# Optimization experiments

Hardware: AMD Instinct MI355X
Metric: run time of the kernel (lower is better)

The kernel has to match this reference:

```python
import jax, jax.numpy as jnp
import numpy as np

D = 2048      # d_model
E = 8         # total experts (0 old + 8 new)
R = 16        # adapter rank
K = 2         # top_k
INIT_BONUS = 3.0
ANNEAL_STEPS = 5000
CURRENT_STEP = 1  # first forward call increments the buffer from 0 to 1


def setup_inputs() -> dict:
    key = jax.random.key(0)
    ks = jax.random.split(key, 7)
    s_in = 1.0 / np.sqrt(D)
    s_r = 1.0 / np.sqrt(R)
    return {
        "x": jax.random.normal(ks[0], (2, 4096, D), dtype=jnp.float32),
        "Wr": jax.random.normal(ks[1], (D, E), dtype=jnp.float32) * s_in,   # router weight
        "br": jax.random.normal(ks[2], (E,), dtype=jnp.float32) * 0.01,     # router bias
        "Wd": jax.random.normal(ks[3], (E, D, R), dtype=jnp.float32) * s_in,  # per-expert down proj
        "bd": jnp.zeros((E, R), dtype=jnp.float32),
        "Wu": jax.random.normal(ks[4], (E, R, D), dtype=jnp.float32) * s_r,   # per-expert up proj
        "bu": jnp.zeros((E, D), dtype=jnp.float32),
    }


def reference(x, Wr, br, Wd, bd, Wu, bu):
    # Router
    logits = jnp.einsum('btd,de->bte', x, Wr) + br
    # Boosted logits (mode='train'): all E experts are new (old_expert_count=0),
    # so the bonus is added to every logit (softmax-invariant here, kept for fidelity).
    progress = min(CURRENT_STEP / ANNEAL_STEPS, 1.0)
    bonus = INIT_BONUS * (1.0 - progress)
    logits = logits + bonus
    gates = jax.nn.softmax(logits, axis=-1)                      # [B,T,E]
    topk_vals, topk_idx = jax.lax.top_k(gates, K)                # [B,T,K]
    topk_vals = topk_vals / topk_vals.sum(axis=-1, keepdims=True)
    # Per-token combine weight for each expert (0 if not in top-k) -- equals the
    # torch loop's weight = (topk_vals * (topk_idx == e)).sum(-1)
    w = (jax.nn.one_hot(topk_idx, E, dtype=x.dtype) * topk_vals[..., None]).sum(axis=-2)  # [B,T,E]
    # Dense per-expert adapter (faithful to the source's dense loop):
    # Adapter(x) = relu(x @ Wd + bd) @ Wu + bu
    h = jax.nn.relu(jnp.einsum('btd,edr->betr', x, Wd) + bd[None, :, None, :])  # [B,E,T,R]
    eo = jnp.einsum('betr,erd->betd', h, Wu) + bu[None, :, None, :]             # [B,E,T,D]
    # Weighted accumulate: output = sum_e w[...,e] * expert_out_e
    out = jnp.einsum('bte,betd->btd', w, eo)                                    # [B,T,D]
    return out
```

## Files before the change

kernel.cpp:

```cpp
#include <hip/hip_runtime.h>
#include <math.h>

#define DMODEL 2048
#define NEXP   8
#define RANK   16
#define NPAIR  28
#define MAXT16 576
#define MAXT32 320

__global__ __launch_bounds__(256, 2)
void router_kernel(const float* __restrict__ x,
                   const float* __restrict__ Wr,
                   const float* __restrict__ br,
                   float2* __restrict__ wparams,
                   int* __restrict__ cnt,
                   unsigned short* __restrict__ lists,
                   int nTok)
{
    __shared__ float wr_lds[DMODEL * NEXP];
    const int tid = threadIdx.x;
    #pragma unroll
    for (int i = 0; i < 16; ++i) {
        const int f = (i*256 + tid)*4;
        *(float4*)&wr_lds[f] = *(const float4*)&Wr[f];
    }
    __syncthreads();

    const int s = tid >> 3;
    const int j = tid & 7;
    const int tok = blockIdx.x*32 + s;
    const bool valid = tok < nTok;
    const float* xr = x + (size_t)(valid ? tok : 0) * DMODEL;

    float part[NEXP];
    #pragma unroll
    for (int e = 0; e < NEXP; ++e) part[e] = 0.f;

    for (int i = 0; i < 64; ++i) {
        const int d0 = (i*8 + j)*4;
        const float4 xv = *(const float4*)&xr[d0];
        #pragma unroll
        for (int q = 0; q < 4; ++q) {
            const float xq = (q==0)?xv.x:(q==1)?xv.y:(q==2)?xv.z:xv.w;
            const float4 w0 = *(const float4*)&wr_lds[(d0+q)*NEXP];
            const float4 w1 = *(const float4*)&wr_lds[(d0+q)*NEXP + 4];
            part[0] = fmaf(xq, w0.x, part[0]);
            part[1] = fmaf(xq, w0.y, part[1]);
            part[2] = fmaf(xq, w0.z, part[2]);
            part[3] = fmaf(xq, w0.w, part[3]);
            part[4] = fmaf(xq, w1.x, part[4]);
            part[5] = fmaf(xq, w1.y, part[5]);
            part[6] = fmaf(xq, w1.z, part[6]);
            part[7] = fmaf(xq, w1.w, part[7]);
        }
    }
    #pragma unroll
    for (int mres = 1; mres < 8; mres <<= 1) {
        #pragma unroll
        for (int e = 0; e < NEXP; ++e)
            part[e] += __shfl_xor(part[e], mres);
    }

    if (j == 0 && valid) {
        float lg[NEXP];
        #pragma unroll
        for (int e = 0; e < NEXP; ++e) lg[e] = part[e] + br[e];
        int b0 = 0; float v0 = lg[0];
        #pragma unroll
        for (int e = 1; e < NEXP; ++e) { if (lg[e] > v0) { v0 = lg[e]; b0 = e; } }
        int b1 = (b0 == 0) ? 1 : 0; float v1 = lg[b1];
        #pragma unroll
        for (int e = 0; e < NEXP; ++e) { if (e != b0 && lg[e] > v1) { v1 = lg[e]; b1 = e; } }
        const float t = expf(v1 - v0);
        const float wtop = 1.f / (1.f + t);
        const float wsec = t / (1.f + t);
        const int lo = (b0 < b1) ? b0 : b1;
        const int hi = (b0 < b1) ? b1 : b0;
        const float wlo = (b0 < b1) ? wtop : wsec;
        const float whi = (b0 < b1) ? wsec : wtop;
        wparams[tok] = make_float2(wlo, whi);
        const int pidx = lo*(NEXP-1) - (lo*(lo-1))/2 + (hi - lo - 1);
        const int pos = atomicAdd(&cnt[pidx], 1);
        lists[(size_t)pidx*nTok + pos] = (unsigned short)tok;
    }
}

__global__ void prefix_kernel(const int* __restrict__ cnt,
                              int* __restrict__ to16,
                              int* __restrict__ to32)
{
    if (threadIdx.x == 0) {
        int a16 = 0, a32 = 0;
        for (int p = 0; p < NPAIR; ++p) {
            to16[p] = a16; to32[p] = a32;
            a16 += (cnt[p] + 15) >> 4;
            a32 += (cnt[p] + 31) >> 5;
        }
        to16[NPAIR] = a16; to32[NPAIR] = a32;
    }
}

__global__ __launch_bounds__(256, 2)
void down_kernel(const float* __restrict__ x,
                 const float* __restrict__ Wd,
                 const float* __restrict__ bd,
                 const float2* __restrict__ wparams,
                 const int* __restrict__ cnt,
                 const int* __restrict__ to16,
                 const unsigned short* __restrict__ lists,
                 float* __restrict__ hw,
                 int nTok)
{
    const int bx = blockIdx.x;
    if (bx >= to16[NPAIR]) return;
    int p = 0;
    while (to16[p+1] <= bx) ++p;
    const int tile = bx - to16[p];
    const int m = min(16, cnt[p] - tile*16);
    int lo = 0, rem = p;
    while (rem >= (NEXP-1-lo)) { rem -= (NEXP-1-lo); ++lo; }
    const int hi = lo + 1 + rem;

    __shared__ float x_lds[16][132];
    __shared__ float wd_lds[2][128][20];
    __shared__ float w_lds[2][16];
    __shared__ int   tok_lds[16];

    const int tid = threadIdx.x;
    if (tid < 16) {
        const int idx = tile*16 + ((tid < m) ? tid : 0);
        const int t = lists[(size_t)p*nTok + idx];
        tok_lds[tid] = t;
        const float2 w = wparams[t];
        w_lds[0][tid] = (tid < m) ? w.x : 0.f;
        w_lds[1][tid] = (tid < m) ? w.y : 0.f;
    }
    __syncthreads();

    const int dg = tid & 31;
    const int kq = tid >> 5;
    const int k  = kq >> 2;
    const int tq = kq & 3;
    const int e  = k ? hi : lo;

    const int sA = tid >> 4;
    const int bA = tid & 15;
    const size_t xbase = (size_t)tok_lds[sA]*DMODEL + bA*8;

    float acc[4][16];
    #pragma unroll
    for (int i = 0; i < 4; ++i)
        #pragma unroll
        for (int r = 0; r < 16; ++r) acc[i][r] = 0.f;

    for (int c = 0; c < 16; ++c) {
        if (c) __syncthreads();
        *(float4*)&x_lds[sA][bA*8]     = *(const float4*)&x[xbase + c*128];
        *(float4*)&x_lds[sA][bA*8 + 4] = *(const float4*)&x[xbase + c*128 + 4];
        #pragma unroll
        for (int o = 0; o < 4; ++o) {
            const int f  = tid*16 + o*4;
            const int kk = f >> 11;
            const int f2 = f & 2047;
            const int es = kk ? hi : lo;
            *(float4*)&wd_lds[kk][f2 >> 4][f2 & 15] =
                *(const float4*)&Wd[(size_t)es*(DMODEL*RANK) + (size_t)c*2048 + f2];
        }
        __syncthreads();
        #pragma unroll
        for (int j = 0; j < 4; ++j) {
            const int d = j*32 + dg;
            const float4 wa = *(const float4*)&wd_lds[k][d][0];
            const float4 wb = *(const float4*)&wd_lds[k][d][4];
            const float4 wc = *(const float4*)&wd_lds[k][d][8];
            const float4 we = *(const float4*)&wd_lds[k][d][12];
            #pragma unroll
            for (int i = 0; i < 4; ++i) {
                const float xv = x_lds[tq*4 + i][d];
                acc[i][0]  = fmaf(xv, wa.x, acc[i][0]);
                acc[i][1]  = fmaf(xv, wa.y, acc[i][1]);
                acc[i][2]  = fmaf(xv, wa.z, acc[i][2]);
                acc[i][3]  = fmaf(xv, wa.w, acc[i][3]);
                acc[i][4]  = fmaf(xv, wb.x, acc[i][4]);
                acc[i][5]  = fmaf(xv, wb.y, acc[i][5]);
                acc[i][6]  = fmaf(xv, wb.z, acc[i][6]);
                acc[i][7]  = fmaf(xv, wb.w, acc[i][7]);
                acc[i][8]  = fmaf(xv, wc.x, acc[i][8]);
                acc[i][9]  = fmaf(xv, wc.y, acc[i][9]);
                acc[i][10] = fmaf(xv, wc.z, acc[i][10]);
                acc[i][11] = fmaf(xv, wc.w, acc[i][11]);
                acc[i][12] = fmaf(xv, we.x, acc[i][12]);
                acc[i][13] = fmaf(xv, we.y, acc[i][13]);
                acc[i][14] = fmaf(xv, we.z, acc[i][14]);
                acc[i][15] = fmaf(xv, we.w, acc[i][15]);
            }
        }
    }

    #pragma unroll
    for (int mm = 1; mm <= 16; mm <<= 1)
        #pragma unroll
        for (int i = 0; i < 4; ++i)
            #pragma unroll
            for (int r = 0; r < 16; ++r)
                acc[i][r] += __shfl_xor(acc[i][r], mm);

    if (dg == 0) {
        #pragma unroll
        for (int i = 0; i < 4; ++i) {
            const int slot = tq*4 + i;
            if (slot < m) {
                const int t = tok_lds[slot];
                const float w = w_lds[k][slot];
                float4 h0, h1, h2, h3;
                h0.x = fmaxf(acc[i][0]  + bd[e*RANK+0],  0.f) * w;
                h0.y = fmaxf(acc[i][1]  + bd[e*RANK+1],  0.f) * w;
                h0.z = fmaxf(acc[i][2]  + bd[e*RANK+2],  0.f) * w;
                h0.w = fmaxf(acc[i][3]  + bd[e*RANK+3],  0.f) * w;
                h1.x = fmaxf(acc[i][4]  + bd[e*RANK+4],  0.f) * w;
                h1.y = fmaxf(acc[i][5]  + bd[e*RANK+5],  0.f) * w;
                h1.z = fmaxf(acc[i][6]  + bd[e*RANK+6],  0.f) * w;
                h1.w = fmaxf(acc[i][7]  + bd[e*RANK+7],  0.f) * w;
                h2.x = fmaxf(acc[i][8]  + bd[e*RANK+8],  0.f) * w;
                h2.y = fmaxf(acc[i][9]  + bd[e*RANK+9],  0.f) * w;
                h2.z = fmaxf(acc[i][10] + bd[e*RANK+10], 0.f) * w;
                h2.w = fmaxf(acc[i][11] + bd[e*RANK+11], 0.f) * w;
                h3.x = fmaxf(acc[i][12] + bd[e*RANK+12], 0.f) * w;
                h3.y = fmaxf(acc[i][13] + bd[e*RANK+13], 0.f) * w;
                h3.z = fmaxf(acc[i][14] + bd[e*RANK+14], 0.f) * w;
                h3.w = fmaxf(acc[i][15] + bd[e*RANK+15], 0.f) * w;
                float* hp = &hw[(size_t)t*32 + k*16];
                *(float4*)&hp[0]  = h0;
                *(float4*)&hp[4]  = h1;
                *(float4*)&hp[8]  = h2;
                *(float4*)&hp[12] = h3;
            }
        }
    }
}

__global__ __launch_bounds__(256, 2)
void up_kernel(const float* __restrict__ Wu,
               const float* __restrict__ bu,
               const float2* __restrict__ wparams,
               const int* __restrict__ cnt,
               const int* __restrict__ to32,
               const unsigned short* __restrict__ lists,
               const float* __restrict__ hw,
               float* __restrict__ out,
               int nTok)
{
    const int bx = blockIdx.x;
    if (bx >= to32[NPAIR]) return;
    int p = 0;
    while (to32[p+1] <= bx) ++p;
    const int tile = bx - to32[p];
    const int m = min(32, cnt[p] - tile*32);
    int lo = 0, rem = p;
    while (rem >= (NEXP-1-lo)) { rem -= (NEXP-1-lo); ++lo; }
    const int hi = lo + 1 + rem;
    const int cc = blockIdx.y;

    __shared__ float wu_lds[2][16][256];
    __shared__ float h_lds[32][36];
    __shared__ float w2_lds[2][32];
    __shared__ int   tok_lds[32];

    const int tid = threadIdx.x;

    if (tid < 32) {
        const int idx = tile*32 + ((tid < m) ? tid : 0);
        const int t = lists[(size_t)p*nTok + idx];
        tok_lds[tid] = t;
        const float2 w = wparams[t];
        w2_lds[0][tid] = (tid < m) ? w.x : 0.f;
        w2_lds[1][tid] = (tid < m) ? w.y : 0.f;
    }

    #pragma unroll
    for (int i = 0; i < 8; ++i) {
        const int f  = i*1024 + tid*4;
        const int kk = f >> 12;
        const int rr = (f >> 8) & 15;
        const int dd = f & 255;
        const int es = kk ? hi : lo;
        *(float4*)&wu_lds[kk][rr][dd] =
            *(const float4*)&Wu[(size_t)es*(RANK*DMODEL) + (size_t)rr*DMODEL + cc*256 + dd];
    }
    __syncthreads();

    {
        const int tk = tid >> 3, o = (tid & 7) * 4;
        const float4 hv = *(const float4*)&hw[(size_t)tok_lds[tk]*32 + o];
        *(float4*)&h_lds[tk][o] = hv;
    }
    __syncthreads();

    const int dg = tid & 31;
    const int tq = tid >> 5;
    float4 a0[4], a1[4];
    #pragma unroll
    for (int i = 0; i < 4; ++i) { a0[i] = make_float4(0,0,0,0); a1[i] = make_float4(0,0,0,0); }

    #pragma unroll 8
    for (int kr = 0; kr < 32; ++kr) {
        const int kk = kr >> 4, rr = kr & 15;
        const float4 u0 = *(const float4*)&wu_lds[kk][rr][dg*4];
        const float4 u1 = *(const float4*)&wu_lds[kk][rr][128 + dg*4];
        #pragma unroll
        for (int i = 0; i < 4; ++i) {
            const float hv = h_lds[tq*4 + i][kr];
            a0[i].x = fmaf(hv, u0.x, a0[i].x);
            a0[i].y = fmaf(hv, u0.y, a0[i].y);
            a0[i].z = fmaf(hv, u0.z, a0[i].z);
            a0[i].w = fmaf(hv, u0.w, a0[i].w);
            a1[i].x = fmaf(hv, u1.x, a1[i].x);
            a1[i].y = fmaf(hv, u1.y, a1[i].y);
            a1[i].z = fmaf(hv, u1.z, a1[i].z);
            a1[i].w = fmaf(hv, u1.w, a1[i].w);
        }
    }

    const float4 bl0 = *(const float4*)&bu[(size_t)lo*DMODEL + cc*256 + dg*4];
    const float4 bl1 = *(const float4*)&bu[(size_t)lo*DMODEL + cc*256 + 128 + dg*4];
    const float4 bh0 = *(const float4*)&bu[(size_t)hi*DMODEL + cc*256 + dg*4];
    const float4 bh1 = *(const float4*)&bu[(size_t)hi*DMODEL + cc*256 + 128 + dg*4];

    #pragma unroll
    for (int i = 0; i < 4; ++i) {
        const int slot = tq*4 + i;
        if (slot < m) {
            const int t = tok_lds[slot];
            const float wl = w2_lds[0][slot];
            const float wh = w2_lds[1][slot];
            float4 o0 = a0[i], o1 = a1[i];
            o0.x += wl*bl0.x + wh*bh0.x;  o0.y += wl*bl0.y + wh*bh0.y;
            o0.z += wl*bl0.z + wh*bh0.z;  o0.w += wl*bl0.w + wh*bh0.w;
            o1.x += wl*bl1.x + wh*bh1.x;  o1.y += wl*bl1.y + wh*bh1.y;
            o1.z += wl*bl1.z + wh*bh1.z;  o1.w += wl*bl1.w + wh*bh1.w;
            float* op = &out[(size_t)t*DMODEL + cc*256];
            *(float4*)&op[dg*4]       = o0;
            *(float4*)&op[128 + dg*4] = o1;
        }
    }
}

extern "C" void kernel_launch(void* const* d_in, const int* in_sizes, int n_in,
                              void* d_out, int out_size, void* d_ws, size_t ws_size,
                              hipStream_t stream)
{
    (void)n_in; (void)out_size; (void)ws_size;
    const float* x  = (const float*)d_in[0];
    const float* Wr = (const float*)d_in[1];
    const float* br = (const float*)d_in[2];
    const float* Wd = (const float*)d_in[3];
    const float* bd = (const float*)d_in[4];
    const float* Wu = (const float*)d_in[5];
    const float* bu = (const float*)d_in[6];
    float* out = (float*)d_out;
    const int nTok = in_sizes[0] / DMODEL;

    char* base = (char*)d_ws;
    int* cnt  = (int*)(base);
    int* to16 = (int*)(base + 128);
    int* to32 = (int*)(base + 256);
    float2* wparams = (float2*)(base + 512);
    size_t off = 512 + (size_t)nTok*sizeof(float2);
    unsigned short* lists = (unsigned short*)(base + off);
    off += (size_t)NPAIR*nTok*sizeof(unsigned short);
    off = (off + 255) & ~(size_t)255;
    float* hw = (float*)(base + off);

    hipMemsetAsync(d_ws, 0, 512, stream);
    const int ntiles = (nTok + 31)/32;
    router_kernel<<<ntiles, 256, 0, stream>>>(x, Wr, br, wparams, cnt, lists, nTok);
    prefix_kernel<<<1, 64, 0, stream>>>(cnt, to16, to32);
    down_kernel<<<MAXT16, 256, 0, stream>>>(x, Wd, bd, wparams, cnt, to16, lists, hw, nTok);
    dim3 gup(MAXT32, 8);
    up_kernel<<<gup, 256, 0, stream>>>(Wu, bu, wparams, cnt, to32, lists, hw, out, nTok);
}
```

Before: 111.6 us.

## Rewrite down projection as per-thread token dot products and transpose router weights

The down-projection kernel drops its LDS-tiled 16-token scheme with cross-lane shuffle reductions. Each thread now owns one token, one expert of the pair and four rank outputs, streaming its x row and Wd directly from global memory over 32-token tiles. The router transposes Wr into an expert-major LDS layout and has each thread handle two tokens, so each weight read is reused across both. This removes LDS staging, barriers and the large shuffle reduction, at the cost of uncoalesced per-thread x row reads and heavy L1/L2 reliance.

Result: slower. 308.9 us (+176.8%).

```diff
diff --git a/kernel.cpp b/kernel.cpp
--- a/kernel.cpp
+++ b/kernel.cpp
@@ -5,7 +5,6 @@
 #define NEXP   8
 #define RANK   16
 #define NPAIR  28
-#define MAXT16 576
 #define MAXT32 320
 
 __global__ __launch_bounds__(256, 2)
@@ -17,86 +16,98 @@
                    unsigned short* __restrict__ lists,
                    int nTok)
 {
-    __shared__ float wr_lds[DMODEL * NEXP];
+    __shared__ float wr_t[NEXP][DMODEL];
     const int tid = threadIdx.x;
     #pragma unroll
     for (int i = 0; i < 16; ++i) {
         const int f = (i*256 + tid)*4;
-        *(float4*)&wr_lds[f] = *(const float4*)&Wr[f];
+        const int d = f >> 3;
+        const int e0 = f & 7;
+        const float4 v = *(const float4*)&Wr[f];
+        wr_t[e0+0][d] = v.x;
+        wr_t[e0+1][d] = v.y;
+        wr_t[e0+2][d] = v.z;
+        wr_t[e0+3][d] = v.w;
     }
     __syncthreads();
 
-    const int s = tid >> 3;
-    const int j = tid & 7;
-    const int tok = blockIdx.x*32 + s;
-    const bool valid = tok < nTok;
-    const float* xr = x + (size_t)(valid ? tok : 0) * DMODEL;
-
-    float part[NEXP];
-    #pragma unroll
-    for (int e = 0; e < NEXP; ++e) part[e] = 0.f;
-
-    for (int i = 0; i < 64; ++i) {
-        const int d0 = (i*8 + j)*4;
-        const float4 xv = *(const float4*)&xr[d0];
+    const int j  = tid & 15;
+    const int su = tid >> 4;
+    const int tok0 = blockIdx.x*32 + su*2;
+    const int tok1 = tok0 + 1;
+    const bool v0 = tok0 < nTok, v1 = tok1 < nTok;
+    const float* xr0 = x + (size_t)(v0 ? tok0 : 0) * DMODEL;
+    const float* xr1 = x + (size_t)(v1 ? tok1 : 0) * DMODEL;
+
+    float pa[NEXP], pb[NEXP];
+    #pragma unroll
+    for (int e = 0; e < NEXP; ++e) { pa[e] = 0.f; pb[e] = 0.f; }
+
+    for (int i = 0; i < 32; ++i) {
+        const int d0 = (i*16 + j)*4;
+        const float4 xa = *(const float4*)&xr0[d0];
+        const float4 xb = *(const float4*)&xr1[d0];
         #pragma unroll
-        for (int q = 0; q < 4; ++q) {
-            const float xq = (q==0)?xv.x:(q==1)?xv.y:(q==2)?xv.z:xv.w;
-            const float4 w0 = *(const float4*)&wr_lds[(d0+q)*NEXP];
-            const float4 w1 = *(const float4*)&wr_lds[(d0+q)*NEXP + 4];
-            part[0] = fmaf(xq, w0.x, part[0]);
-            part[1] = fmaf(xq, w0.y, part[1]);
-            part[2] = fmaf(xq, w0.z, part[2]);
-            part[3] = fmaf(xq, w0.w, part[3]);
-            part[4] = fmaf(xq, w1.x, part[4]);
-            part[5] = fmaf(xq, w1.y, part[5]);
-            part[6] = fmaf(xq, w1.z, part[6]);
-            part[7] = fmaf(xq, w1.w, part[7]);
-        }
-    }
-    #pragma unroll
-    for (int mres = 1; mres < 8; mres <<= 1) {
+        for (int e = 0; e < NEXP; ++e) {
+            const float4 wv = *(const float4*)&wr_t[e][d0];
+            pa[e] = fmaf(xa.x, wv.x, pa[e]);
+            pa[e] = fmaf(xa.y, wv.y, pa[e]);
+            pa[e] = fmaf(xa.z, wv.z, pa[e]);
+            pa[e] = fmaf(xa.w, wv.w, pa[e]);
+            pb[e] = fmaf(xb.x, wv.x, pb[e]);
+            pb[e] = fmaf(xb.y, wv.y, pb[e]);
+            pb[e] = fmaf(xb.z, wv.z, pb[e]);
+            pb[e] = fmaf(xb.w, wv.w, pb[e]);
+        }
+    }
+    #pragma unroll
+    for (int mres = 1; mres < 16; mres <<= 1) {
         #pragma unroll
-        for (int e = 0; e < NEXP; ++e)
-            part[e] += __shfl_xor(part[e], mres);
-    }
-
-    if (j == 0 && valid) {
-        float lg[NEXP];
+        for (int e = 0; e < NEXP; ++e) {
+            pa[e] += __shfl_xor(pa[e], mres);
+            pb[e] += __shfl_xor(pb[e], mres);
+        }
+    }
+
+    if (j == 0) {
         #pragma unroll
-        for (int e = 0; e < NEXP; ++e) lg[e] = part[e] + br[e];
-        int b0 = 0; float v0 = lg[0];
-        #pragma unroll
-        for (int e = 1; e < NEXP; ++e) { if (lg[e] > v0) { v0 = lg[e]; b0 = e; } }
-        int b1 = (b0 == 0) ? 1 : 0; float v1 = lg[b1];
-        #pragma unroll
-        for (int e = 0; e < NEXP; ++e) { if (e != b0 && lg[e] > v1) { v1 = lg[e]; b1 = e; } }
-        const float t = expf(v1 - v0);
-        const float wtop = 1.f / (1.f + t);
-        const float wsec = t / (1.f + t);
-        const int lo = (b0 < b1) ? b0 : b1;
-        const int hi = (b0 < b1) ? b1 : b0;
-        const float wlo = (b0 < b1) ? wtop : wsec;
-        const float whi = (b0 < b1) ? wsec : wtop;
-        wparams[tok] = make_float2(wlo, whi);
-        const int pidx = lo*(NEXP-1) - (lo*(lo-1))/2 + (hi - lo - 1);
-        const int pos = atomicAdd(&cnt[pidx], 1);
-        lists[(size_t)pidx*nTok + pos] = (unsigned short)tok;
+        for (int tt = 0; tt < 2; ++tt) {
+            const int tok = tt ? tok1 : tok0;
+            if (tok >= nTok) continue;
+            float lg[NEXP];
+            #pragma unroll
+            for (int e = 0; e < NEXP; ++e) lg[e] = (tt ? pb[e] : pa[e]) + br[e];
+            int b0 = 0; float w0 = lg[0];
+            #pragma unroll
+            for (int e = 1; e < NEXP; ++e) { if (lg[e] > w0) { w0 = lg[e]; b0 = e; } }
+            int b1 = (b0 == 0) ? 1 : 0; float w1 = lg[b1];
+            #pragma unroll
+            for (int e = 0; e < NEXP; ++e) { if (e != b0 && lg[e] > w1) { w1 = lg[e]; b1 = e; } }
+            const float t = expf(w1 - w0);
+            const float wtop = 1.f / (1.f + t);
+            const float wsec = t / (1.f + t);
+            const int lo = (b0 < b1) ? b0 : b1;
+            const int hi = (b0 < b1) ? b1 : b0;
+            const float wlo = (b0 < b1) ? wtop : wsec;
+            const float whi = (b0 < b1) ? wsec : wtop;
+            wparams[tok] = make_float2(wlo, whi);
+            const int pidx = lo*(NEXP-1) - (lo*(lo-1))/2 + (hi - lo - 1);
+            const int pos = atomicAdd(&cnt[pidx], 1);
+            lists[(size_t)pidx*nTok + pos] = (unsigned short)tok;
+        }
     }
 }
 
 __global__ void prefix_kernel(const int* __restrict__ cnt,
-                              int* __restrict__ to16,
                               int* __restrict__ to32)
 {
     if (threadIdx.x == 0) {
-        int a16 = 0, a32 = 0;
+        int a32 = 0;
         for (int p = 0; p < NPAIR; ++p) {
-            to16[p] = a16; to32[p] = a32;
-            a16 += (cnt[p] + 15) >> 4;
+            to32[p] = a32;
             a32 += (cnt[p] + 31) >> 5;
         }
-        to16[NPAIR] = a16; to32[NPAIR] = a32;
+        to32[NPAIR] = a32;
     }
 }
 
@@ -105,137 +116,62 @@
                  const float* __restrict__ Wd,
                  const float* __restrict__ bd,
                  const float2* __restrict__ wparams,
+                 const int* __restrict__ to32,
                  const int* __restrict__ cnt,
-                 const int* __restrict__ to16,
                  const unsigned short* __restrict__ lists,
                  float* __restrict__ hw,
                  int nTok)
 {
     const int bx = blockIdx.x;
-    if (bx >= to16[NPAIR]) return;
+    if (bx >= to32[NPAIR]) return;
     int p = 0;
-    while (to16[p+1] <= bx) ++p;
-    const int tile = bx - to16[p];
-    const int m = min(16, cnt[p] - tile*16);
+    while (to32[p+1] <= bx) ++p;
+    const int tile = bx - to32[p];
+    const int m = min(32, cnt[p] - tile*32);
     int lo = 0, rem = p;
     while (rem >= (NEXP-1-lo)) { rem -= (NEXP-1-lo); ++lo; }
     const int hi = lo + 1 + rem;
 
-    __shared__ float x_lds[16][132];
-    __shared__ float wd_lds[2][128][20];
-    __shared__ float w_lds[2][16];
-    __shared__ int   tok_lds[16];
-
     const int tid = threadIdx.x;
-    if (tid < 16) {
-        const int idx = tile*16 + ((tid < m) ? tid : 0);
-        const int t = lists[(size_t)p*nTok + idx];
-        tok_lds[tid] = t;
-        const float2 w = wparams[t];
-        w_lds[0][tid] = (tid < m) ? w.x : 0.f;
-        w_lds[1][tid] = (tid < m) ? w.y : 0.f;
-    }
-    __syncthreads();
-
-    const int dg = tid & 31;
-    const int kq = tid >> 5;
-    const int k  = kq >> 2;
-    const int tq = kq & 3;
+    const int ts = tid & 31;
+    const int k  = (tid >> 5) & 1;
+    const int rq = tid >> 6;
     const int e  = k ? hi : lo;
-
-    const int sA = tid >> 4;
-    const int bA = tid & 15;
-    const size_t xbase = (size_t)tok_lds[sA]*DMODEL + bA*8;
-
-    float acc[4][16];
-    #pragma unroll
-    for (int i = 0; i < 4; ++i)
-        #pragma unroll
-        for (int r = 0; r < 16; ++r) acc[i][r] = 0.f;
-
-    for (int c = 0; c < 16; ++c) {
-        if (c) __syncthreads();
-        *(float4*)&x_lds[sA][bA*8]     = *(const float4*)&x[xbase + c*128];
-        *(float4*)&x_lds[sA][bA*8 + 4] = *(const float4*)&x[xbase + c*128 + 4];
-        #pragma unroll
-        for (int o = 0; o < 4; ++o) {
-            const int f  = tid*16 + o*4;
-            const int kk = f >> 11;
-            const int f2 = f & 2047;
-            const int es = kk ? hi : lo;
-            *(float4*)&wd_lds[kk][f2 >> 4][f2 & 15] =
-                *(const float4*)&Wd[(size_t)es*(DMODEL*RANK) + (size_t)c*2048 + f2];
-        }
-        __syncthreads();
-        #pragma unroll
-        for (int j = 0; j < 4; ++j) {
-            const int d = j*32 + dg;
-            const float4 wa = *(const float4*)&wd_lds[k][d][0];
-            const float4 wb = *(const float4*)&wd_lds[k][d][4];
-            const float4 wc = *(const float4*)&wd_lds[k][d][8];
-            const float4 we = *(const float4*)&wd_lds[k][d][12];
-            #pragma unroll
-            for (int i = 0; i < 4; ++i) {
-                const float xv = x_lds[tq*4 + i][d];
-                acc[i][0]  = fmaf(xv, wa.x, acc[i][0]);
-                acc[i][1]  = fmaf(xv, wa.y, acc[i][1]);
-                acc[i][2]  = fmaf(xv, wa.z, acc[i][2]);
-                acc[i][3]  = fmaf(xv, wa.w, acc[i][3]);
-                acc[i][4]  = fmaf(xv, wb.x, acc[i][4]);
-                acc[i][5]  = fmaf(xv, wb.y, acc[i][5]);
-                acc[i][6]  = fmaf(xv, wb.z, acc[i][6]);
-                acc[i][7]  = fmaf(xv, wb.w, acc[i][7]);
-                acc[i][8]  = fmaf(xv, wc.x, acc[i][8]);
-                acc[i][9]  = fmaf(xv, wc.y, acc[i][9]);
-                acc[i][10] = fmaf(xv, wc.z, acc[i][10]);
-                acc[i][11] = fmaf(xv, wc.w, acc[i][11]);
-                acc[i][12] = fmaf(xv, we.x, acc[i][12]);
-                acc[i][13] = fmaf(xv, we.y, acc[i][13]);
-                acc[i][14] = fmaf(xv, we.z, acc[i][14]);
-                acc[i][15] = fmaf(xv, we.w, acc[i][15]);
-            }
-        }
-    }
-
-    #pragma unroll
-    for (int mm = 1; mm <= 16; mm <<= 1)
-        #pragma unroll
-        for (int i = 0; i < 4; ++i)
-            #pragma unroll
-            for (int r = 0; r < 16; ++r)
-                acc[i][r] += __shfl_xor(acc[i][r], mm);
-
-    if (dg == 0) {
-        #pragma unroll
-        for (int i = 0; i < 4; ++i) {
-            const int slot = tq*4 + i;
-            if (slot < m) {
-                const int t = tok_lds[slot];
-                const float w = w_lds[k][slot];
-                float4 h0, h1, h2, h3;
-                h0.x = fmaxf(acc[i][0]  + bd[e*RANK+0],  0.f) * w;
-                h0.y = fmaxf(acc[i][1]  + bd[e*RANK+1],  0.f) * w;
-                h0.z = fmaxf(acc[i][2]  + bd[e*RANK+2],  0.f) * w;
-                h0.w = fmaxf(acc[i][3]  + bd[e*RANK+3],  0.f) * w;
-                h1.x = fmaxf(acc[i][4]  + bd[e*RANK+4],  0.f) * w;
-                h1.y = fmaxf(acc[i][5]  + bd[e*RANK+5],  0.f) * w;
-                h1.z = fmaxf(acc[i][6]  + bd[e*RANK+6],  0.f) * w;
-                h1.w = fmaxf(acc[i][7]  + bd[e*RANK+7],  0.f) * w;
-                h2.x = fmaxf(acc[i][8]  + bd[e*RANK+8],  0.f) * w;
-                h2.y = fmaxf(acc[i][9]  + bd[e*RANK+9],  0.f) * w;
-                h2.z = fmaxf(acc[i][10] + bd[e*RANK+10], 0.f) * w;
-                h2.w = fmaxf(acc[i][11] + bd[e*RANK+11], 0.f) * w;
-                h3.x = fmaxf(acc[i][12] + bd[e*RANK+12], 0.f) * w;
-                h3.y = fmaxf(acc[i][13] + bd[e*RANK+13], 0.f) * w;
-                h3.z = fmaxf(acc[i][14] + bd[e*RANK+14], 0.f) * w;
-                h3.w = fmaxf(acc[i][15] + bd[e*RANK+15], 0.f) * w;
-                float* hp = &hw[(size_t)t*32 + k*16];
-                *(float4*)&hp[0]  = h0;
-                *(float4*)&hp[4]  = h1;
-                *(float4*)&hp[8]  = h2;
-                *(float4*)&hp[12] = h3;
-            }
-        }
+    const bool valid = ts < m;
+    const int tok = lists[(size_t)p*nTok + tile*32 + (valid ? ts : 0)];
+
+    const float* xp = x + (size_t)tok * DMODEL;
+    const float* wp = Wd + (size_t)e * (DMODEL*RANK) + rq*4;
+
+    float ax = 0.f, ay = 0.f, az = 0.f, aw = 0.f;
+    #pragma unroll 4
+    for (int dc = 0; dc < DMODEL/4; ++dc) {
+        const int d = dc*4;
+        const float4 xv = *(const float4*)&xp[d];
+        const float4 w0 = *(const float4*)&wp[(d+0)*RANK];
+        const float4 w1 = *(const float4*)&wp[(d+1)*RANK];
+        const float4 w2 = *(const float4*)&wp[(d+2)*RANK];
+        const float4 w3 = *(const float4*)&wp[(d+3)*RANK];
+        ax = fmaf(xv.x, w0.x, ax); ax = fmaf(xv.y, w1.x, ax);
+        ax = fmaf(xv.z, w2.x, ax); ax = fmaf(xv.w, w3.x, ax);
+        ay = fmaf(xv.x, w0.y, ay); ay = fmaf(xv.y, w1.y, ay);
+        ay = fmaf(xv.z, w2.y, ay); ay = fmaf(xv.w, w3.y, ay);
+        az = fmaf(xv.x, w0.z, az); az = fmaf(xv.y, w1.z, az);
+        az = fmaf(xv.z, w2.z, az); az = fmaf(xv.w, w3.z, az);
+        aw = fmaf(xv.x, w0.w, aw); aw = fmaf(xv.y, w1.w, aw);
+        aw = fmaf(xv.z, w2.w, aw); aw = fmaf(xv.w, w3.w, aw);
+    }
+
+    const float2 wp2 = wparams[tok];
+    const float w = k ? wp2.y : wp2.x;
+    const float4 bdv = *(const float4*)&bd[e*RANK + rq*4];
+    float4 h;
+    h.x = fmaxf(ax + bdv.x, 0.f) * w;
+    h.y = fmaxf(ay + bdv.y, 0.f) * w;
+    h.z = fmaxf(az + bdv.z, 0.f) * w;
+    h.w = fmaxf(aw + bdv.w, 0.f) * w;
+    if (valid) {
+        *(float4*)&hw[(size_t)tok*32 + k*16 + rq*4] = h;
     }
 }
 
@@ -362,7 +298,6 @@
 
     char* base = (char*)d_ws;
     int* cnt  = (int*)(base);
-    int* to16 = (int*)(base + 128);
     int* to32 = (int*)(base + 256);
     float2* wparams = (float2*)(base + 512);
     size_t off = 512 + (size_t)nTok*sizeof(float2);
@@ -374,8 +309,8 @@
     hipMemsetAsync(d_ws, 0, 512, stream);
     const int ntiles = (nTok + 31)/32;
     router_kernel<<<ntiles, 256, 0, stream>>>(x, Wr, br, wparams, cnt, lists, nTok);
-    prefix_kernel<<<1, 64, 0, stream>>>(cnt, to16, to32);
-    down_kernel<<<MAXT16, 256, 0, stream>>>(x, Wd, bd, wparams, cnt, to16, lists, hw, nTok);
+    prefix_kernel<<<1, 64, 0, stream>>>(cnt, to32);
+    down_kernel<<<MAXT32, 256, 0, stream>>>(x, Wd, bd, wparams, to32, cnt, lists, hw, nTok);
     dim3 gup(MAXT32, 8);
     up_kernel<<<gup, 256, 0, stream>>>(Wu, bu, wparams, cnt, to32, lists, hw, out, nTok);
 }
```

## Restructure router and split down-projection over two D halves

Applied to the files above, without the earlier changes.

The router drops its 64KB LDS staging of Wr. Each block now handles 16 tokens, each warp-group covers two experts, and Wr and x are read straight from global memory. The down kernel adds a grid dimension that splits D into two halves and reads x and Wd directly without LDS tiles or barriers, writing partial sums to a wider hw2 buffer. The up kernel then adds the two partials, applies bias, ReLU and the gate weight. The aim is more parallelism and occupancy in the router and down stages; the cost is uncoalesced scalar x gathers and extra partial-sum traffic.

Measured after the change: 149.4 us. 33.9% more time.

```diff
diff --git a/kernel.cpp b/kernel.cpp
--- a/kernel.cpp
+++ b/kernel.cpp
@@ -17,71 +17,76 @@
                    unsigned short* __restrict__ lists,
                    int nTok)
 {
-    __shared__ float wr_lds[DMODEL * NEXP];
+    __shared__ float lg_lds[16][8];
+
     const int tid = threadIdx.x;
-    #pragma unroll
-    for (int i = 0; i < 16; ++i) {
-        const int f = (i*256 + tid)*4;
-        *(float4*)&wr_lds[f] = *(const float4*)&Wr[f];
+    const int dg  = tid & 31;
+    const int grp = tid >> 5;
+    const int ep  = grp & 3;
+    const int th  = grp >> 2;
+    const int tbase = blockIdx.x*16 + th*8;
+
+    float a0[8], a1[8];
+    #pragma unroll
+    for (int t = 0; t < 8; ++t) { a0[t] = 0.f; a1[t] = 0.f; }
+
+    for (int it = 0; it < 16; ++it) {
+        const int d0 = it*128 + dg*4;
+        const float2 w0 = *(const float2*)&Wr[(d0+0)*NEXP + ep*2];
+        const float2 w1 = *(const float2*)&Wr[(d0+1)*NEXP + ep*2];
+        const float2 w2 = *(const float2*)&Wr[(d0+2)*NEXP + ep*2];
+        const float2 w3 = *(const float2*)&Wr[(d0+3)*NEXP + ep*2];
+        #pragma unroll
+        for (int t = 0; t < 8; ++t) {
+            const float4 xv = *(const float4*)&x[(size_t)(tbase+t)*DMODEL + d0];
+            a0[t] = fmaf(xv.x, w0.x, a0[t]);
+            a0[t] = fmaf(xv.y, w1.x, a0[t]);
+            a0[t] = fmaf(xv.z, w2.x, a0[t]);
+            a0[t] = fmaf(xv.w, w3.x, a0[t]);
+            a1[t] = fmaf(xv.x, w0.y, a1[t]);
+            a1[t] = fmaf(xv.y, w1.y, a1[t]);
+            a1[t] = fmaf(xv.z, w2.y, a1[t]);
+            a1[t] = fmaf(xv.w, w3.y, a1[t]);
+        }
+    }
+    #pragma unroll
+    for (int mm = 1; mm <= 16; mm <<= 1) {
+        #pragma unroll
+        for (int t = 0; t < 8; ++t) {
+            a0[t] += __shfl_xor(a0[t], mm);
+            a1[t] += __shfl_xor(a1[t], mm);
+        }
+    }
+    if (dg < 8) {
+        lg_lds[th*8 + dg][ep*2 + 0] = a0[dg];
+        lg_lds[th*8 + dg][ep*2 + 1] = a1[dg];
     }
     __syncthreads();
 
-    const int s = tid >> 3;
-    const int j = tid & 7;
-    const int tok = blockIdx.x*32 + s;
-    const bool valid = tok < nTok;
-    const float* xr = x + (size_t)(valid ? tok : 0) * DMODEL;
-
-    float part[NEXP];
-    #pragma unroll
-    for (int e = 0; e < NEXP; ++e) part[e] = 0.f;
-
-    for (int i = 0; i < 64; ++i) {
-        const int d0 = (i*8 + j)*4;
-        const float4 xv = *(const float4*)&xr[d0];
-        #pragma unroll
-        for (int q = 0; q < 4; ++q) {
-            const float xq = (q==0)?xv.x:(q==1)?xv.y:(q==2)?xv.z:xv.w;
-            const float4 w0 = *(const float4*)&wr_lds[(d0+q)*NEXP];
-            const float4 w1 = *(const float4*)&wr_lds[(d0+q)*NEXP + 4];
-            part[0] = fmaf(xq, w0.x, part[0]);
-            part[1] = fmaf(xq, w0.y, part[1]);
-            part[2] = fmaf(xq, w0.z, part[2]);
-            part[3] = fmaf(xq, w0.w, part[3]);
-            part[4] = fmaf(xq, w1.x, part[4]);
-            part[5] = fmaf(xq, w1.y, part[5]);
-            part[6] = fmaf(xq, w1.z, part[6]);
-            part[7] = fmaf(xq, w1.w, part[7]);
-        }
-    }
-    #pragma unroll
-    for (int mres = 1; mres < 8; mres <<= 1) {
-        #pragma unroll
-        for (int e = 0; e < NEXP; ++e)
-            part[e] += __shfl_xor(part[e], mres);
-    }
-
-    if (j == 0 && valid) {
-        float lg[NEXP];
-        #pragma unroll
-        for (int e = 0; e < NEXP; ++e) lg[e] = part[e] + br[e];
-        int b0 = 0; float v0 = lg[0];
-        #pragma unroll
-        for (int e = 1; e < NEXP; ++e) { if (lg[e] > v0) { v0 = lg[e]; b0 = e; } }
-        int b1 = (b0 == 0) ? 1 : 0; float v1 = lg[b1];
-        #pragma unroll
-        for (int e = 0; e < NEXP; ++e) { if (e != b0 && lg[e] > v1) { v1 = lg[e]; b1 = e; } }
-        const float t = expf(v1 - v0);
-        const float wtop = 1.f / (1.f + t);
-        const float wsec = t / (1.f + t);
-        const int lo = (b0 < b1) ? b0 : b1;
-        const int hi = (b0 < b1) ? b1 : b0;
-        const float wlo = (b0 < b1) ? wtop : wsec;
-        const float whi = (b0 < b1) ? wsec : wtop;
-        wparams[tok] = make_float2(wlo, whi);
-        const int pidx = lo*(NEXP-1) - (lo*(lo-1))/2 + (hi - lo - 1);
-        const int pos = atomicAdd(&cnt[pidx], 1);
-        lists[(size_t)pidx*nTok + pos] = (unsigned short)tok;
+    if (tid < 16) {
+        const int tok = blockIdx.x*16 + tid;
+        if (tok < nTok) {
+            float lg[NEXP];
+            #pragma unroll
+            for (int e = 0; e < NEXP; ++e) lg[e] = lg_lds[tid][e] + br[e];
+            int b0 = 0; float v0 = lg[0];
+            #pragma unroll
+            for (int e = 1; e < NEXP; ++e) { if (lg[e] > v0) { v0 = lg[e]; b0 = e; } }
+            int b1 = (b0 == 0) ? 1 : 0; float v1 = lg[b1];
+            #pragma unroll
+            for (int e = 0; e < NEXP; ++e) { if (e != b0 && lg[e] > v1) { v1 = lg[e]; b1 = e; } }
+            const float t = expf(v1 - v0);
+            const float wtop = 1.f / (1.f + t);
+            const float wsec = t / (1.f + t);
+            const int lo = (b0 < b1) ? b0 : b1;
+            const int hi = (b0 < b1) ? b1 : b0;
+            const float wlo = (b0 < b1) ? wtop : wsec;
+            const float whi = (b0 < b1) ? wsec : wtop;
+            wparams[tok] = make_float2(wlo, whi);
+            const int pidx = lo*(NEXP-1) - (lo*(lo-1))/2 + (hi - lo - 1);
+            const int pos = atomicAdd(&cnt[pidx], 1);
+            lists[(size_t)pidx*nTok + pos] = (unsigned short)tok;
+        }
     }
 }
 
@@ -103,12 +108,10 @@
 __global__ __launch_bounds__(256, 2)
 void down_kernel(const float* __restrict__ x,
                  const float* __restrict__ Wd,
-                 const float* __restrict__ bd,
-                 const float2* __restrict__ wparams,
                  const int* __restrict__ cnt,
                  const int* __restrict__ to16,
                  const unsigned short* __restrict__ lists,
-                 float* __restrict__ hw,
+                 float* __restrict__ hw2,
                  int nTok)
 {
     const int bx = blockIdx.x;
@@ -120,32 +123,22 @@
     int lo = 0, rem = p;
     while (rem >= (NEXP-1-lo)) { rem -= (NEXP-1-lo); ++lo; }
     const int hi = lo + 1 + rem;
-
-    __shared__ float x_lds[16][132];
-    __shared__ float wd_lds[2][128][20];
-    __shared__ float w_lds[2][16];
-    __shared__ int   tok_lds[16];
+    const int ch = blockIdx.y;
 
     const int tid = threadIdx.x;
-    if (tid < 16) {
-        const int idx = tile*16 + ((tid < m) ? tid : 0);
-        const int t = lists[(size_t)p*nTok + idx];
-        tok_lds[tid] = t;
-        const float2 w = wparams[t];
-        w_lds[0][tid] = (tid < m) ? w.x : 0.f;
-        w_lds[1][tid] = (tid < m) ? w.y : 0.f;
-    }
-    __syncthreads();
-
     const int dg = tid & 31;
-    const int kq = tid >> 5;
-    const int k  = kq >> 2;
-    const int tq = kq & 3;
+    const int tq = (tid >> 5) & 3;
+    const int k  = tid >> 7;
     const int e  = k ? hi : lo;
 
-    const int sA = tid >> 4;
-    const int bA = tid & 15;
-    const size_t xbase = (size_t)tok_lds[sA]*DMODEL + bA*8;
+    int toks[4];
+    #pragma unroll
+    for (int i = 0; i < 4; ++i) {
+        const int slot = tq*4 + i;
+        toks[i] = lists[(size_t)p*nTok + tile*16 + ((slot < m) ? slot : 0)];
+    }
+
+    const float* wdp = Wd + (size_t)e * (DMODEL*RANK);
 
     float acc[4][16];
     #pragma unroll
@@ -153,47 +146,35 @@
         #pragma unroll
         for (int r = 0; r < 16; ++r) acc[i][r] = 0.f;
 
-    for (int c = 0; c < 16; ++c) {
-        if (c) __syncthreads();
-        *(float4*)&x_lds[sA][bA*8]     = *(const float4*)&x[xbase + c*128];
-        *(float4*)&x_lds[sA][bA*8 + 4] = *(const float4*)&x[xbase + c*128 + 4];
-        #pragma unroll
-        for (int o = 0; o < 4; ++o) {
-            const int f  = tid*16 + o*4;
-            const int kk = f >> 11;
-            const int f2 = f & 2047;
-            const int es = kk ? hi : lo;
-            *(float4*)&wd_lds[kk][f2 >> 4][f2 & 15] =
-                *(const float4*)&Wd[(size_t)es*(DMODEL*RANK) + (size_t)c*2048 + f2];
-        }
-        __syncthreads();
-        #pragma unroll
-        for (int j = 0; j < 4; ++j) {
-            const int d = j*32 + dg;
-            const float4 wa = *(const float4*)&wd_lds[k][d][0];
-            const float4 wb = *(const float4*)&wd_lds[k][d][4];
-            const float4 wc = *(const float4*)&wd_lds[k][d][8];
-            const float4 we = *(const float4*)&wd_lds[k][d][12];
-            #pragma unroll
-            for (int i = 0; i < 4; ++i) {
-                const float xv = x_lds[tq*4 + i][d];
-                acc[i][0]  = fmaf(xv, wa.x, acc[i][0]);
-                acc[i][1]  = fmaf(xv, wa.y, acc[i][1]);
-                acc[i][2]  = fmaf(xv, wa.z, acc[i][2]);
-                acc[i][3]  = fmaf(xv, wa.w, acc[i][3]);
-                acc[i][4]  = fmaf(xv, wb.x, acc[i][4]);
-                acc[i][5]  = fmaf(xv, wb.y, acc[i][5]);
-                acc[i][6]  = fmaf(xv, wb.z, acc[i][6]);
-                acc[i][7]  = fmaf(xv, wb.w, acc[i][7]);
-                acc[i][8]  = fmaf(xv, wc.x, acc[i][8]);
-                acc[i][9]  = fmaf(xv, wc.y, acc[i][9]);
-                acc[i][10] = fmaf(xv, wc.z, acc[i][10]);
-                acc[i][11] = fmaf(xv, wc.w, acc[i][11]);
-                acc[i][12] = fmaf(xv, we.x, acc[i][12]);
-                acc[i][13] = fmaf(xv, we.y, acc[i][13]);
-                acc[i][14] = fmaf(xv, we.z, acc[i][14]);
-                acc[i][15] = fmaf(xv, we.w, acc[i][15]);
-            }
+    const int dbase = ch*1024 + dg;
+    #pragma unroll 2
+    for (int jj = 0; jj < 32; ++jj) {
+        const int d = dbase + jj*32;
+        const float4 w0 = *(const float4*)&wdp[d*RANK + 0];
+        const float4 w1 = *(const float4*)&wdp[d*RANK + 4];
+        const float4 w2 = *(const float4*)&wdp[d*RANK + 8];
+        const float4 w3 = *(const float4*)&wdp[d*RANK + 12];
+        float xv[4];
+        #pragma unroll
+        for (int i = 0; i < 4; ++i) xv[i] = x[(size_t)toks[i]*DMODEL + d];
+        #pragma unroll
+        for (int i = 0; i < 4; ++i) {
+            acc[i][0]  = fmaf(xv[i], w0.x, acc[i][0]);
+            acc[i][1]  = fmaf(xv[i], w0.y, acc[i][1]);
+            acc[i][2]  = fmaf(xv[i], w0.z, acc[i][2]);
+            acc[i][3]  = fmaf(xv[i], w0.w, acc[i][3]);
+            acc[i][4]  = fmaf(xv[i], w1.x, acc[i][4]);
+            acc[i][5]  = fmaf(xv[i], w1.y, acc[i][5]);
+            acc[i][6]  = fmaf(xv[i], w1.z, acc[i][6]);
+            acc[i][7]  = fmaf(xv[i], w1.w, acc[i][7]);
+            acc[i][8]  = fmaf(xv[i], w2.x, acc[i][8]);
+            acc[i][9]  = fmaf(xv[i], w2.y, acc[i][9]);
+            acc[i][10] = fmaf(xv[i], w2.z, acc[i][10]);
+            acc[i][11] = fmaf(xv[i], w2.w, acc[i][11]);
+            acc[i][12] = fmaf(xv[i], w3.x, acc[i][12]);
+            acc[i][13] = fmaf(xv[i], w3.y, acc[i][13]);
+            acc[i][14] = fmaf(xv[i], w3.z, acc[i][14]);
+            acc[i][15] = fmaf(xv[i], w3.w, acc[i][15]);
         }
     }
 
@@ -205,36 +186,17 @@
             for (int r = 0; r < 16; ++r)
                 acc[i][r] += __shfl_xor(acc[i][r], mm);
 
-    if (dg == 0) {
-        #pragma unroll
-        for (int i = 0; i < 4; ++i) {
-            const int slot = tq*4 + i;
-            if (slot < m) {
-                const int t = tok_lds[slot];
-                const float w = w_lds[k][slot];
-                float4 h0, h1, h2, h3;
-                h0.x = fmaxf(acc[i][0]  + bd[e*RANK+0],  0.f) * w;
-                h0.y = fmaxf(acc[i][1]  + bd[e*RANK+1],  0.f) * w;
-                h0.z = fmaxf(acc[i][2]  + bd[e*RANK+2],  0.f) * w;
-                h0.w = fmaxf(acc[i][3]  + bd[e*RANK+3],  0.f) * w;
-                h1.x = fmaxf(acc[i][4]  + bd[e*RANK+4],  0.f) * w;
-                h1.y = fmaxf(acc[i][5]  + bd[e*RANK+5],  0.f) * w;
-                h1.z = fmaxf(acc[i][6]  + bd[e*RANK+6],  0.f) * w;
-                h1.w = fmaxf(acc[i][7]  + bd[e*RANK+7],  0.f) * w;
-                h2.x = fmaxf(acc[i][8]  + bd[e*RANK+8],  0.f) * w;
-                h2.y = fmaxf(acc[i][9]  + bd[e*RANK+9],  0.f) * w;
-                h2.z = fmaxf(acc[i][10] + bd[e*RANK+10], 0.f) * w;
-                h2.w = fmaxf(acc[i][11] + bd[e*RANK+11], 0.f) * w;
-                h3.x = fmaxf(acc[i][12] + bd[e*RANK+12], 0.f) * w;
-                h3.y = fmaxf(acc[i][13] + bd[e*RANK+13], 0.f) * w;
-                h3.z = fmaxf(acc[i][14] + bd[e*RANK+14], 0.f) * w;
-                h3.w = fmaxf(acc[i][15] + bd[e*RANK+15], 0.f) * w;
-                float* hp = &hw[(size_t)t*32 + k*16];
-                *(float4*)&hp[0]  = h0;
-                *(float4*)&hp[4]  = h1;
-                *(float4*)&hp[8]  = h2;
-                *(float4*)&hp[12] = h3;
-            }
+    if (dg < 16) {
+        const int i  = dg >> 2;
+        const int rq = dg & 3;
+        const int slot = tq*4 + i;
+        if (slot < m) {
+            float4 v;
+            v.x = acc[i][rq*4+0];
+            v.y = acc[i][rq*4+1];
+            v.z = acc[i][rq*4+2];
+            v.w = acc[i][rq*4+3];
+            *(float4*)&hw2[(size_t)toks[i]*64 + ch*32 + k*16 + rq*4] = v;
         }
     }
 }
@@ -242,11 +204,12 @@
 __global__ __launch_bounds__(256, 2)
 void up_kernel(const float* __restrict__ Wu,
                const float* __restrict__ bu,
+               const float* __restrict__ bd,
                const float2* __restrict__ wparams,
                const int* __restrict__ cnt,
                const int* __restrict__ to32,
                const unsigned short* __restrict__ lists,
-               const float* __restrict__ hw,
+               const float* __restrict__ hw2,
                float* __restrict__ out,
                int nTok)
 {
@@ -290,9 +253,21 @@
     __syncthreads();
 
     {
-        const int tk = tid >> 3, o = (tid & 7) * 4;
-        const float4 hv = *(const float4*)&hw[(size_t)tok_lds[tk]*32 + o];
-        *(float4*)&h_lds[tk][o] = hv;
+        const int t8 = tid >> 3;
+        const int kk = (tid >> 2) & 1;
+        const int rq = tid & 3;
+        const int e2 = kk ? hi : lo;
+        const float* hp = &hw2[(size_t)tok_lds[t8]*64 + kk*16 + rq*4];
+        const float4 s0 = *(const float4*)&hp[0];
+        const float4 s1 = *(const float4*)&hp[32];
+        const float4 bdv = *(const float4*)&bd[e2*RANK + rq*4];
+        const float w = w2_lds[kk][t8];
+        float4 h;
+        h.x = fmaxf(s0.x + s1.x + bdv.x, 0.f) * w;
+        h.y = fmaxf(s0.y + s1.y + bdv.y, 0.f) * w;
+        h.z = fmaxf(s0.z + s1.z + bdv.z, 0.f) * w;
+        h.w = fmaxf(s0.w + s1.w + bdv.w, 0.f) * w;
+        *(float4*)&h_lds[t8][kk*16 + rq*4] = h;
     }
     __syncthreads();
 
@@ -369,13 +344,14 @@
     unsigned short* lists = (unsigned short*)(base + off);
     off += (size_t)NPAIR*nTok*sizeof(unsigned short);
     off = (off + 255) & ~(size_t)255;
-    float* hw = (float*)(base + off);
+    float* hw2 = (float*)(base + off);
 
     hipMemsetAsync(d_ws, 0, 512, stream);
-    const int ntiles = (nTok + 31)/32;
-    router_kernel<<<ntiles, 256, 0, stream>>>(x, Wr, br, wparams, cnt, lists, nTok);
+    const int ntiles16 = (nTok + 15)/16;
+    router_kernel<<<ntiles16, 256, 0, stream>>>(x, Wr, br, wparams, cnt, lists, nTok);
     prefix_kernel<<<1, 64, 0, stream>>>(cnt, to16, to32);
-    down_kernel<<<MAXT16, 256, 0, stream>>>(x, Wd, bd, wparams, cnt, to16, lists, hw, nTok);
+    dim3 gdown(MAXT16, 2);
+    down_kernel<<<gdown, 256, 0, stream>>>(x, Wd, cnt, to16, lists, hw2, nTok);
     dim3 gup(MAXT32, 8);
-    up_kernel<<<gup, 256, 0, stream>>>(Wu, bu, wparams, cnt, to32, lists, hw, out, nTok);
-}
+    up_kernel<<<gup, 256, 0, stream>>>(Wu, bu, bd, wparams, cnt, to32, lists, hw2, out, nTok);
+}
```
